# Kernel optimization log

Hardware: AMD Instinct MI355X
Metric: run time of the kernel (lower is better)

The kernel has to match this reference:

```python
import jax, jax.numpy as jnp
import numpy as np

EMBED = 1024
HEADS = 16

def setup_inputs() -> dict:
    key = jax.random.key(0)
    ks = jax.random.split(key, 6)
    N, S = 1, 4096
    half = EMBED // 2
    x = jax.random.normal(ks[0], (N, S, EMBED), dtype=jnp.float32)
    Wq = jax.random.normal(ks[1], (half, half), dtype=jnp.float32) * 0.02
    Wk = jax.random.normal(ks[2], (half, half), dtype=jnp.float32) * 0.02
    Wv = jax.random.normal(ks[3], (half, half), dtype=jnp.float32) * 0.02
    Wo = jax.random.normal(ks[4], (EMBED, half), dtype=jnp.float32) * 0.02
    bo = jnp.zeros((EMBED,), dtype=jnp.float32)
    return {"x": x, "Wq": Wq, "Wk": Wk, "Wv": Wv, "Wo": Wo, "bo": bo}

def reference(x, Wq, Wk, Wv, Wo, bo):
    N, S, E = x.shape
    H = HEADS
    Dh = (E // 2) // H                 # per-head dim of the half-width projections (32)
    scale = float(E // H) ** 0.5       # original scales by head_dim = embed/heads = 64
    left = x[..., : E // 2]            # only the left chunk feeds attention in the source
    # torch Linear: y = x @ W.T (no bias)
    q = (left @ Wq.T).reshape(N, S, H, Dh)
    k = (left @ Wk.T).reshape(N, S, H, Dh)
    v = (left @ Wv.T).reshape(N, S, H, Dh)
    energy = jnp.einsum('nqhd,nkhd->nqkh', q, k)          # [N,S,S,H] full score tensor
    att = jax.nn.softmax(energy / scale, axis=2)          # softmax over key axis
    out = jnp.einsum('nqkh,nkhd->nqhd', att, v)           # [N,S,H,Dh]
    out = out.reshape(N, S, E // 2)
    return out @ Wo.T + bo                                # fc_out: half -> embed
```

## Files before the change

### kernel.cpp

```cpp
#include <hip/hip_runtime.h>
#include <stdint.h>


#define SEQ    4096
#define DMODEL 1024
#define DHALF  512
#define NH     16
#define DH     32

typedef __attribute__((ext_vector_type(4))) float facc4;
typedef __attribute__((ext_vector_type(8))) short bfrag8;

#define MFMA_BF16(a, b, c) __builtin_amdgcn_mfma_f32_16x16x32_bf16((a), (b), (c), 0, 0, 0)

static __device__ __forceinline__ uint16_t f2b(float x) {
    uint32_t u = __float_as_uint(x);
    return (uint16_t)((u + 0x7FFFu + ((u >> 16) & 1u)) >> 16);
}
static __device__ __forceinline__ float b2f(uint16_t b) {
    return __uint_as_float(((uint32_t)b) << 16);
}

static __device__ __forceinline__ bfrag8 cvt8perm(float4 a, float4 b) {
    uint32_t u0 = __float_as_uint(a.x) + 0x8000u, u1 = __float_as_uint(a.y) + 0x8000u;
    uint32_t u2 = __float_as_uint(a.z) + 0x8000u, u3 = __float_as_uint(a.w) + 0x8000u;
    uint32_t u4 = __float_as_uint(b.x) + 0x8000u, u5 = __float_as_uint(b.y) + 0x8000u;
    uint32_t u6 = __float_as_uint(b.z) + 0x8000u, u7 = __float_as_uint(b.w) + 0x8000u;
    union { uint32_t w[4]; bfrag8 r; } u;
    u.w[0] = __builtin_amdgcn_perm(u1, u0, 0x07060302u);
    u.w[1] = __builtin_amdgcn_perm(u3, u2, 0x07060302u);
    u.w[2] = __builtin_amdgcn_perm(u5, u4, 0x07060302u);
    u.w[3] = __builtin_amdgcn_perm(u7, u6, 0x07060302u);
    return u.r;
}

__global__ __launch_bounds__(256) void convert_w(
    const float* __restrict__ Wq, const float* __restrict__ Wk,
    const float* __restrict__ Wv, const float* __restrict__ Wo,
    uint16_t* __restrict__ q, uint16_t* __restrict__ k,
    uint16_t* __restrict__ v, uint16_t* __restrict__ o)
{
    int zz = blockIdx.x;
    const float* src; uint16_t* dst; size_t off;
    if      (zz < 128) { src = Wq; dst = q; off = (size_t)zz * 2048; }
    else if (zz < 256) { src = Wk; dst = k; off = (size_t)(zz - 128) * 2048; }
    else if (zz < 384) { src = Wv; dst = v; off = (size_t)(zz - 256) * 2048; }
    else               { src = Wo; dst = o; off = (size_t)(zz - 384) * 2048; }
    size_t i = off + (size_t)threadIdx.x * 8;
    float4 a = *(const float4*)&src[i];
    float4 b = *(const float4*)&src[i + 4];
    *(bfrag8*)&dst[i] = cvt8perm(a, b);
}

template <int AF32>
__device__ __forceinline__ void gemm128T(
    const void* __restrict__ A, int lda,
    const uint16_t* __restrict__ B, int ldb,
    void* __restrict__ C, int ldc, int cF32,
    const float* __restrict__ bias, float scale,
    int Kd, int m0, int n0)
{
    __shared__ __align__(16) uint16_t As[2][128 * 40];
    __shared__ __align__(16) uint16_t Bs[2][128 * 40];

    const int tid  = threadIdx.x;
    const int lane = tid & 63;
    const int wv   = tid >> 6;
    const int lo   = lane & 15;
    const int quad = lane >> 4;
    const int srow = tid >> 2;
    const int skq  = (tid & 3) * 8;
    const int rb   = (wv >> 1) * 64;
    const int cb   = (wv & 1) * 64;

    const facc4 ZACC = {0.f, 0.f, 0.f, 0.f};
    facc4 acc[4][4];
#pragma unroll
    for (int i = 0; i < 4; ++i)
#pragma unroll
        for (int j = 0; j < 4; ++j) acc[i][j] = ZACC;

    const float*    fA0 = AF32 ? &((const float*)A)[(size_t)(m0 + srow) * lda + skq] : nullptr;
    const float*    fA1 = AF32 ? &((const float*)A)[(size_t)(m0 + srow + 64) * lda + skq] : nullptr;
    const uint16_t* hA0 = AF32 ? nullptr : &((const uint16_t*)A)[(size_t)(m0 + srow) * lda + skq];
    const uint16_t* hA1 = AF32 ? nullptr : &((const uint16_t*)A)[(size_t)(m0 + srow + 64) * lda + skq];
    const uint16_t* pB0 = &B[(size_t)(n0 + srow) * ldb + skq];
    const uint16_t* pB1 = &B[(size_t)(n0 + srow + 64) * ldb + skq];

    bfrag8 ra0, ra1;
    float4 f0a, f0b, f1a, f1b;
    if (AF32) {
        f0a = *(const float4*)fA0; f0b = *(const float4*)(fA0 + 4);
        f1a = *(const float4*)fA1; f1b = *(const float4*)(fA1 + 4);
    } else {
        ra0 = *(const bfrag8*)hA0;
        ra1 = *(const bfrag8*)hA1;
    }
    bfrag8 rb0 = *(const bfrag8*)pB0;
    bfrag8 rb1 = *(const bfrag8*)pB1;

    if (AF32) {
        *(bfrag8*)&As[0][srow * 40 + skq]        = cvt8perm(f0a, f0b);
        *(bfrag8*)&As[0][(srow + 64) * 40 + skq] = cvt8perm(f1a, f1b);
    } else {
        *(bfrag8*)&As[0][srow * 40 + skq]        = ra0;
        *(bfrag8*)&As[0][(srow + 64) * 40 + skq] = ra1;
    }
    *(bfrag8*)&Bs[0][srow * 40 + skq]        = rb0;
    *(bfrag8*)&Bs[0][(srow + 64) * 40 + skq] = rb1;
    __syncthreads();

    int p = 0;
    for (int kt = 0; kt < Kd; kt += 32) {
        const bool more = (kt + 32 < Kd);
        if (more) {
            if (AF32) {
                f0a = *(const float4*)(fA0 + kt + 32); f0b = *(const float4*)(fA0 + kt + 36);
                f1a = *(const float4*)(fA1 + kt + 32); f1b = *(const float4*)(fA1 + kt + 36);
            } else {
                ra0 = *(const bfrag8*)(hA0 + kt + 32);
                ra1 = *(const bfrag8*)(hA1 + kt + 32);
            }
            rb0 = *(const bfrag8*)(pB0 + kt + 32);
            rb1 = *(const bfrag8*)(pB1 + kt + 32);
        }

        bfrag8 af[4], bf[4];
#pragma unroll
        for (int i = 0; i < 4; ++i) {
            af[i] = *(const bfrag8*)&As[p][(rb + i * 16 + lo) * 40 + quad * 8];
            bf[i] = *(const bfrag8*)&Bs[p][(cb + i * 16 + lo) * 40 + quad * 8];
        }
#pragma unroll
        for (int i = 0; i < 4; ++i)
#pragma unroll
            for (int j = 0; j < 4; ++j)
                acc[i][j] = MFMA_BF16(af[i], bf[j], acc[i][j]);

        if (more) {
            if (AF32) {
                *(bfrag8*)&As[1 - p][srow * 40 + skq]        = cvt8perm(f0a, f0b);
                *(bfrag8*)&As[1 - p][(srow + 64) * 40 + skq] = cvt8perm(f1a, f1b);
            } else {
                *(bfrag8*)&As[1 - p][srow * 40 + skq]        = ra0;
                *(bfrag8*)&As[1 - p][(srow + 64) * 40 + skq] = ra1;
            }
            *(bfrag8*)&Bs[1 - p][srow * 40 + skq]        = rb0;
            *(bfrag8*)&Bs[1 - p][(srow + 64) * 40 + skq] = rb1;
            __syncthreads();
            p ^= 1;
        }
    }

#pragma unroll
    for (int j = 0; j < 4; ++j) {
        int col  = n0 + cb + j * 16 + lo;
        float bv = bias ? bias[col] : 0.f;
#pragma unroll
        for (int i = 0; i < 4; ++i) {
#pragma unroll
            for (int r = 0; r < 4; ++r) {
                int row = m0 + rb + i * 16 + quad * 4 + r;
                float v = acc[i][j][r] * scale + bv;
                if (cF32) ((float*)C)[(size_t)row * ldc + col] = v;
                else      ((uint16_t*)C)[(size_t)row * ldc + col] = f2b(v);
            }
        }
    }
}

#define SC_Q (0.125f * 1.4426950408889634f)

__global__ __launch_bounds__(256, 2) void qkv_kernel(
    const float* __restrict__ x,
    const uint16_t* __restrict__ Wqb, const uint16_t* __restrict__ Wkb,
    const uint16_t* __restrict__ Wvb,
    uint16_t* __restrict__ Q, uint16_t* __restrict__ K, uint16_t* __restrict__ V)
{
    const int z = blockIdx.z;
    const uint16_t* W = (z == 0) ? Wqb : (z == 1) ? Wkb : Wvb;
    uint16_t* Out     = (z == 0) ? Q   : (z == 1) ? K   : V;
    float scale       = (z == 0) ? SC_Q : 1.0f;
    gemm128T<1>(x, DMODEL, W, DHALF, Out, DHALF, 0, nullptr, scale, DHALF,
                blockIdx.y * 128, blockIdx.x * 128);
}

__global__ __launch_bounds__(256, 2) void outproj_kernel(
    const uint16_t* __restrict__ O, const uint16_t* __restrict__ Wob,
    const float* __restrict__ bo, float* __restrict__ Y)
{
    gemm128T<0>(O, DHALF, Wob, DHALF, Y, DMODEL, 1, bo, 1.0f, DHALF,
                blockIdx.y * 128, blockIdx.x * 128);
}

__global__ __launch_bounds__(256) void attn_kernel(
    const uint16_t* __restrict__ Q, const uint16_t* __restrict__ Kb,
    const uint16_t* __restrict__ Vb, uint16_t* __restrict__ Op,
    float* __restrict__ lbuf, int kspan)
{
    __shared__ __align__(16) uint16_t Ks[64 * 40];
    __shared__ __align__(16) uint16_t Vt[32 * 64];
    __shared__ __align__(16) uint16_t Ps[4 * 16 * 72];

    const int tid  = threadIdx.x;
    const int lane = tid & 63;
    const int wv   = tid >> 6;
    const int lo   = lane & 15;
    const int quad = lane >> 4;
    const int h    = blockIdx.y;
    const int q0   = blockIdx.x * 64;
    const int sp   = blockIdx.z;
    const int srow = tid >> 2;
    const int skq  = (tid & 3) * 8;

    const facc4 ZACC = {0.f, 0.f, 0.f, 0.f};

    const bfrag8 qf = *(const bfrag8*)&Q[(size_t)(q0 + wv * 16 + lo) * DHALF + h * DH + quad * 8];

    bfrag8 ones;
#pragma unroll
    for (int j = 0; j < 8; ++j) ones[j] = (short)0x3F80;

    int vt_w[8];
#pragma unroll
    for (int j = 0; j < 8; ++j) {
        int d  = skq + j;
        int Rd = ((d & 7) + 2 * (d >> 3)) & 7;
        vt_w[j] = d * 64 + ((((srow >> 3) + Rd) & 7) << 3) + (srow & 7);
    }
    int vt_r[2][2];
#pragma unroll
    for (int dt = 0; dt < 2; ++dt) {
        int d  = dt * 16 + lo;
        int Rd = ((d & 7) + 2 * (d >> 3)) & 7;
#pragma unroll
        for (int c = 0; c < 2; ++c)
            vt_r[c][dt] = d * 64 + ((((c * 4 + quad) + Rd) & 7) << 3);
    }
    const int pbase = wv * (16 * 72);
    const int ps_w  = pbase + lo * 72 + 4 * quad;
    const int ps_r  = pbase + lo * 72 + quad * 8;
    const int ks_r  = lo * 40 + quad * 8;

    const uint16_t* pK = &Kb[(size_t)srow * DHALF + h * DH + skq];
    const uint16_t* pV = &Vb[(size_t)srow * DHALF + h * DH + skq];

    facc4 oacc[2], oaccL;
    oacc[0] = ZACC; oacc[1] = ZACC; oaccL = ZACC;

    const int kb0  = sp * kspan;
    const int kend = kb0 + kspan;

    float4 kreg = *(const float4*)(pK + (size_t)kb0 * DHALF);
    float4 vreg = *(const float4*)(pV + (size_t)kb0 * DHALF);

    for (int kb = kb0; kb < kend; kb += 64) {
        *(float4*)&Ks[srow * 40 + skq] = kreg;
        {
            const uint16_t* vp = (const uint16_t*)&vreg;
#pragma unroll
            for (int j = 0; j < 8; ++j) Vt[vt_w[j]] = vp[j];
        }
        __syncthreads();

        if (kb + 64 < kend) {
            kreg = *(const float4*)(pK + (size_t)(kb + 64) * DHALF);
            vreg = *(const float4*)(pV + (size_t)(kb + 64) * DHALF);
        }

#pragma unroll
        for (int t = 0; t < 4; ++t) {
            bfrag8 kf = *(const bfrag8*)&Ks[t * 640 + ks_r];
            facc4 s = MFMA_BF16(kf, qf, ZACC);
            float p0 = __builtin_amdgcn_exp2f(s[0]);
            float p1 = __builtin_amdgcn_exp2f(s[1]);
            float p2 = __builtin_amdgcn_exp2f(s[2]);
            float p3 = __builtin_amdgcn_exp2f(s[3]);
            uint32_t u0 = __float_as_uint(p0) + 0x8000u;
            uint32_t u1 = __float_as_uint(p1) + 0x8000u;
            uint32_t u2 = __float_as_uint(p2) + 0x8000u;
            uint32_t u3 = __float_as_uint(p3) + 0x8000u;
            uint2 w;
            w.x = __builtin_amdgcn_perm(u1, u0, 0x07060302u);
            w.y = __builtin_amdgcn_perm(u3, u2, 0x07060302u);
            *(uint2*)&Ps[ps_w + 16 * t] = w;
        }
        __builtin_amdgcn_wave_barrier();

#pragma unroll
        for (int c = 0; c < 2; ++c) {
            bfrag8 pf = *(const bfrag8*)&Ps[ps_r + c * 32];
#pragma unroll
            for (int dt = 0; dt < 2; ++dt) {
                bfrag8 vf = *(const bfrag8*)&Vt[vt_r[c][dt]];
                oacc[dt] = MFMA_BF16(pf, vf, oacc[dt]);
            }
            oaccL = MFMA_BF16(pf, ones, oaccL);
        }
        __syncthreads();
    }

    if (lo == 0) {
#pragma unroll
        for (int r = 0; r < 4; ++r)
            lbuf[((size_t)sp * NH + h) * SEQ + q0 + wv * 16 + quad * 4 + r] = oaccL[r];
    }

    uint16_t* Od = Op + (size_t)sp * SEQ * DHALF;
#pragma unroll
    for (int r = 0; r < 4; ++r) {
        int row = q0 + wv * 16 + quad * 4 + r;
        Od[(size_t)row * DHALF + h * DH + lo]      = f2b(oacc[0][r]);
        Od[(size_t)row * DHALF + h * DH + 16 + lo] = f2b(oacc[1][r]);
    }
}

__global__ __launch_bounds__(256) void combine_kernel(
    const uint16_t* __restrict__ Op, const float* __restrict__ lbuf,
    uint16_t* __restrict__ O, int ns)
{
    int t   = blockIdx.x * 256 + threadIdx.x;
    int row = t >> 6;
    int cb  = (t & 63) << 3;
    int h   = cb >> 5;
    float l = 0.f;
    float acc[8] = {0.f, 0.f, 0.f, 0.f, 0.f, 0.f, 0.f, 0.f};
    for (int sp = 0; sp < ns; ++sp) {
        l += lbuf[((size_t)sp * NH + h) * SEQ + row];
        bfrag8 a = *(const bfrag8*)&Op[(size_t)sp * SEQ * DHALF + (size_t)row * DHALF + cb];
#pragma unroll
        for (int j = 0; j < 8; ++j) acc[j] += b2f((uint16_t)a[j]);
    }
    float inv = 1.0f / l;
    bfrag8 o;
#pragma unroll
    for (int j = 0; j < 8; ++j) o[j] = (short)f2b(acc[j] * inv);
    *(bfrag8*)&O[(size_t)row * DHALF + cb] = o;
}

extern "C" void kernel_launch(void* const* d_in, const int* in_sizes, int n_in,
                              void* d_out, int out_size, void* d_ws, size_t ws_size,
                              hipStream_t stream)
{
    const float* x  = (const float*)d_in[0];
    const float* Wq = (const float*)d_in[1];
    const float* Wk = (const float*)d_in[2];
    const float* Wv = (const float*)d_in[3];
    const float* Wo = (const float*)d_in[4];
    const float* bo = (const float*)d_in[5];

    size_t fixed_e = 3 * (size_t)DHALF * DHALF + (size_t)DMODEL * DHALF
                   + 4 * (size_t)SEQ * DHALF;
    size_t need4 = (fixed_e + 4 * (size_t)SEQ * DHALF) * 2
                 + 4 * (size_t)NH * SEQ * 4;
    const int ns = (ws_size >= need4) ? 4 : 2;

    uint16_t* Wqb = (uint16_t*)d_ws;
    uint16_t* Wkb = Wqb + (size_t)DHALF * DHALF;
    uint16_t* Wvb = Wkb + (size_t)DHALF * DHALF;
    uint16_t* Wob = Wvb + (size_t)DHALF * DHALF;
    uint16_t* Q   = Wob + (size_t)DMODEL * DHALF;
    uint16_t* K   = Q + (size_t)SEQ * DHALF;
    uint16_t* V   = K + (size_t)SEQ * DHALF;
    uint16_t* O   = V + (size_t)SEQ * DHALF;
    uint16_t* Op  = O + (size_t)SEQ * DHALF;
    float*  lbuf  = (float*)(Op + (size_t)ns * SEQ * DHALF);

    convert_w<<<640, 256, 0, stream>>>(Wq, Wk, Wv, Wo, Wqb, Wkb, Wvb, Wob);
    qkv_kernel<<<dim3(DHALF / 128, SEQ / 128, 3), 256, 0, stream>>>(
        x, Wqb, Wkb, Wvb, Q, K, V);
    attn_kernel<<<dim3(SEQ / 64, NH, ns), 256, 0, stream>>>(Q, K, V, Op, lbuf, SEQ / ns);
    combine_kernel<<<1024, 256, 0, stream>>>(Op, lbuf, O, ns);
    outproj_kernel<<<dim3(DMODEL / 128, SEQ / 128), 256, 0, stream>>>(
        O, Wob, bo, (float*)d_out);
}
```

Baseline: 194.5 us.

## Fuse weight conversion and split-K combine into the GEMM tile loaders

Removes the separate weight-conversion kernel by loading fp32 weights directly in the GEMMs and converting them to bf16 while staging to shared memory. Removes the combine kernel by having the output-projection GEMM sum the split attention partials and normalize them by the summed softmax denominators as it stages its A tiles. This saves two launches and the intermediate O buffer. In exchange, the fp32 weight loads double B traffic per tile, and the combine work is redone by every column block of the output GEMM (8 times) inside its staging path.

```diff
diff --git a/kernel.cpp b/kernel.cpp
--- a/kernel.cpp
+++ b/kernel.cpp
@@ -34,31 +34,14 @@
     return u.r;
 }
 
-__global__ __launch_bounds__(256) void convert_w(
-    const float* __restrict__ Wq, const float* __restrict__ Wk,
-    const float* __restrict__ Wv, const float* __restrict__ Wo,
-    uint16_t* __restrict__ q, uint16_t* __restrict__ k,
-    uint16_t* __restrict__ v, uint16_t* __restrict__ o)
-{
-    int zz = blockIdx.x;
-    const float* src; uint16_t* dst; size_t off;
-    if      (zz < 128) { src = Wq; dst = q; off = (size_t)zz * 2048; }
-    else if (zz < 256) { src = Wk; dst = k; off = (size_t)(zz - 128) * 2048; }
-    else if (zz < 384) { src = Wv; dst = v; off = (size_t)(zz - 256) * 2048; }
-    else               { src = Wo; dst = o; off = (size_t)(zz - 384) * 2048; }
-    size_t i = off + (size_t)threadIdx.x * 8;
-    float4 a = *(const float4*)&src[i];
-    float4 b = *(const float4*)&src[i + 4];
-    *(bfrag8*)&dst[i] = cvt8perm(a, b);
-}
-
-template <int AF32>
+template <int AMODE, int BF32>
 __device__ __forceinline__ void gemm128T(
     const void* __restrict__ A, int lda,
-    const uint16_t* __restrict__ B, int ldb,
+    const void* __restrict__ B, int ldb,
     void* __restrict__ C, int ldc, int cF32,
     const float* __restrict__ bias, float scale,
-    int Kd, int m0, int n0)
+    int Kd, int m0, int n0,
+    const float* __restrict__ lbuf, int ns)
 {
     __shared__ __align__(16) uint16_t As[2][128 * 40];
     __shared__ __align__(16) uint16_t Bs[2][128 * 40];
@@ -80,50 +63,82 @@
 #pragma unroll
         for (int j = 0; j < 4; ++j) acc[i][j] = ZACC;
 
-    const float*    fA0 = AF32 ? &((const float*)A)[(size_t)(m0 + srow) * lda + skq] : nullptr;
-    const float*    fA1 = AF32 ? &((const float*)A)[(size_t)(m0 + srow + 64) * lda + skq] : nullptr;
-    const uint16_t* hA0 = AF32 ? nullptr : &((const uint16_t*)A)[(size_t)(m0 + srow) * lda + skq];
-    const uint16_t* hA1 = AF32 ? nullptr : &((const uint16_t*)A)[(size_t)(m0 + srow + 64) * lda + skq];
-    const uint16_t* pB0 = &B[(size_t)(n0 + srow) * ldb + skq];
-    const uint16_t* pB1 = &B[(size_t)(n0 + srow + 64) * ldb + skq];
-
-    bfrag8 ra0, ra1;
-    float4 f0a, f0b, f1a, f1b;
-    if (AF32) {
-        f0a = *(const float4*)fA0; f0b = *(const float4*)(fA0 + 4);
-        f1a = *(const float4*)fA1; f1b = *(const float4*)(fA1 + 4);
-    } else {
-        ra0 = *(const bfrag8*)hA0;
-        ra1 = *(const bfrag8*)hA1;
-    }
-    bfrag8 rb0 = *(const bfrag8*)pB0;
-    bfrag8 rb1 = *(const bfrag8*)pB1;
-
-    if (AF32) {
-        *(bfrag8*)&As[0][srow * 40 + skq]        = cvt8perm(f0a, f0b);
-        *(bfrag8*)&As[0][(srow + 64) * 40 + skq] = cvt8perm(f1a, f1b);
-    } else {
-        *(bfrag8*)&As[0][srow * 40 + skq]        = ra0;
-        *(bfrag8*)&As[0][(srow + 64) * 40 + skq] = ra1;
-    }
-    *(bfrag8*)&Bs[0][srow * 40 + skq]        = rb0;
-    *(bfrag8*)&Bs[0][(srow + 64) * 40 + skq] = rb1;
+    bfrag8 a_b[2]; float4 a_f[2][2];
+    bfrag8 b_b[2]; float4 b_f[2][2];
+
+    auto fetchA = [&](int kt) {
+        if constexpr (AMODE == 0) {
+#pragma unroll
+            for (int hf = 0; hf < 2; ++hf)
+                a_b[hf] = *(const bfrag8*)&((const uint16_t*)A)
+                    [(size_t)(m0 + srow + hf * 64) * lda + kt + skq];
+        } else if constexpr (AMODE == 1) {
+#pragma unroll
+            for (int hf = 0; hf < 2; ++hf) {
+                const float* p = &((const float*)A)
+                    [(size_t)(m0 + srow + hf * 64) * lda + kt + skq];
+                a_f[hf][0] = *(const float4*)p;
+                a_f[hf][1] = *(const float4*)(p + 4);
+            }
+        }
+    };
+    auto fetchB = [&](int kt) {
+#pragma unroll
+        for (int hf = 0; hf < 2; ++hf) {
+            if constexpr (BF32) {
+                const float* p = &((const float*)B)
+                    [(size_t)(n0 + srow + hf * 64) * ldb + kt + skq];
+                b_f[hf][0] = *(const float4*)p;
+                b_f[hf][1] = *(const float4*)(p + 4);
+            } else {
+                b_b[hf] = *(const bfrag8*)&((const uint16_t*)B)
+                    [(size_t)(n0 + srow + hf * 64) * ldb + kt + skq];
+            }
+        }
+    };
+    auto stage = [&](int kt, int buf) {
+#pragma unroll
+        for (int hf = 0; hf < 2; ++hf) {
+            bfrag8 av;
+            if constexpr (AMODE == 0) {
+                av = a_b[hf];
+            } else if constexpr (AMODE == 1) {
+                av = cvt8perm(a_f[hf][0], a_f[hf][1]);
+            } else {
+                size_t row = (size_t)(m0 + srow + hf * 64);
+                int h = kt >> 5;
+                float s[8] = {0.f,0.f,0.f,0.f,0.f,0.f,0.f,0.f};
+                float l = 0.f;
+                for (int sp = 0; sp < ns; ++sp) {
+                    bfrag8 v = *(const bfrag8*)&((const uint16_t*)A)
+                        [(size_t)sp * SEQ * DHALF + row * lda + kt + skq];
+                    l += lbuf[((size_t)sp * NH + h) * SEQ + row];
+#pragma unroll
+                    for (int j = 0; j < 8; ++j) s[j] += b2f((uint16_t)v[j]);
+                }
+                float inv = 1.0f / l;
+                float4 x0 = {s[0]*inv, s[1]*inv, s[2]*inv, s[3]*inv};
+                float4 x1 = {s[4]*inv, s[5]*inv, s[6]*inv, s[7]*inv};
+                av = cvt8perm(x0, x1);
+            }
+            *(bfrag8*)&As[buf][(srow + hf * 64) * 40 + skq] = av;
+
+            bfrag8 bv;
+            if constexpr (BF32) bv = cvt8perm(b_f[hf][0], b_f[hf][1]);
+            else                bv = b_b[hf];
+            *(bfrag8*)&Bs[buf][(srow + hf * 64) * 40 + skq] = bv;
+        }
+    };
+
+    fetchA(0);
+    fetchB(0);
+    stage(0, 0);
     __syncthreads();
 
     int p = 0;
     for (int kt = 0; kt < Kd; kt += 32) {
         const bool more = (kt + 32 < Kd);
-        if (more) {
-            if (AF32) {
-                f0a = *(const float4*)(fA0 + kt + 32); f0b = *(const float4*)(fA0 + kt + 36);
-                f1a = *(const float4*)(fA1 + kt + 32); f1b = *(const float4*)(fA1 + kt + 36);
-            } else {
-                ra0 = *(const bfrag8*)(hA0 + kt + 32);
-                ra1 = *(const bfrag8*)(hA1 + kt + 32);
-            }
-            rb0 = *(const bfrag8*)(pB0 + kt + 32);
-            rb1 = *(const bfrag8*)(pB1 + kt + 32);
-        }
+        if (more) { fetchA(kt + 32); fetchB(kt + 32); }
 
         bfrag8 af[4], bf[4];
 #pragma unroll
@@ -138,15 +153,7 @@
                 acc[i][j] = MFMA_BF16(af[i], bf[j], acc[i][j]);
 
         if (more) {
-            if (AF32) {
-                *(bfrag8*)&As[1 - p][srow * 40 + skq]        = cvt8perm(f0a, f0b);
-                *(bfrag8*)&As[1 - p][(srow + 64) * 40 + skq] = cvt8perm(f1a, f1b);
-            } else {
-                *(bfrag8*)&As[1 - p][srow * 40 + skq]        = ra0;
-                *(bfrag8*)&As[1 - p][(srow + 64) * 40 + skq] = ra1;
-            }
-            *(bfrag8*)&Bs[1 - p][srow * 40 + skq]        = rb0;
-            *(bfrag8*)&Bs[1 - p][(srow + 64) * 40 + skq] = rb1;
+            stage(kt + 32, 1 - p);
             __syncthreads();
             p ^= 1;
         }
@@ -173,24 +180,25 @@
 
 __global__ __launch_bounds__(256, 2) void qkv_kernel(
     const float* __restrict__ x,
-    const uint16_t* __restrict__ Wqb, const uint16_t* __restrict__ Wkb,
-    const uint16_t* __restrict__ Wvb,
+    const float* __restrict__ Wq, const float* __restrict__ Wk,
+    const float* __restrict__ Wv,
     uint16_t* __restrict__ Q, uint16_t* __restrict__ K, uint16_t* __restrict__ V)
 {
     const int z = blockIdx.z;
-    const uint16_t* W = (z == 0) ? Wqb : (z == 1) ? Wkb : Wvb;
-    uint16_t* Out     = (z == 0) ? Q   : (z == 1) ? K   : V;
-    float scale       = (z == 0) ? SC_Q : 1.0f;
-    gemm128T<1>(x, DMODEL, W, DHALF, Out, DHALF, 0, nullptr, scale, DHALF,
-                blockIdx.y * 128, blockIdx.x * 128);
+    const float* W = (z == 0) ? Wq : (z == 1) ? Wk : Wv;
+    uint16_t* Out  = (z == 0) ? Q  : (z == 1) ? K  : V;
+    float scale    = (z == 0) ? SC_Q : 1.0f;
+    gemm128T<1, 1>(x, DMODEL, W, DHALF, Out, DHALF, 0, nullptr, scale, DHALF,
+                   blockIdx.y * 128, blockIdx.x * 128, nullptr, 0);
 }
 
 __global__ __launch_bounds__(256, 2) void outproj_kernel(
-    const uint16_t* __restrict__ O, const uint16_t* __restrict__ Wob,
-    const float* __restrict__ bo, float* __restrict__ Y)
-{
-    gemm128T<0>(O, DHALF, Wob, DHALF, Y, DMODEL, 1, bo, 1.0f, DHALF,
-                blockIdx.y * 128, blockIdx.x * 128);
+    const uint16_t* __restrict__ Op, const float* __restrict__ Wo,
+    const float* __restrict__ bo, float* __restrict__ Y,
+    const float* __restrict__ lbuf, int ns)
+{
+    gemm128T<2, 1>(Op, DHALF, Wo, DHALF, Y, DMODEL, 1, bo, 1.0f, DHALF,
+                   blockIdx.y * 128, blockIdx.x * 128, lbuf, ns);
 }
 
 __global__ __launch_bounds__(256) void attn_kernel(
@@ -315,29 +323,6 @@
     }
 }
 
-__global__ __launch_bounds__(256) void combine_kernel(
-    const uint16_t* __restrict__ Op, const float* __restrict__ lbuf,
-    uint16_t* __restrict__ O, int ns)
-{
-    int t   = blockIdx.x * 256 + threadIdx.x;
-    int row = t >> 6;
-    int cb  = (t & 63) << 3;
-    int h   = cb >> 5;
-    float l = 0.f;
-    float acc[8] = {0.f, 0.f, 0.f, 0.f, 0.f, 0.f, 0.f, 0.f};
-    for (int sp = 0; sp < ns; ++sp) {
-        l += lbuf[((size_t)sp * NH + h) * SEQ + row];
-        bfrag8 a = *(const bfrag8*)&Op[(size_t)sp * SEQ * DHALF + (size_t)row * DHALF + cb];
-#pragma unroll
-        for (int j = 0; j < 8; ++j) acc[j] += b2f((uint16_t)a[j]);
-    }
-    float inv = 1.0f / l;
-    bfrag8 o;
-#pragma unroll
-    for (int j = 0; j < 8; ++j) o[j] = (short)f2b(acc[j] * inv);
-    *(bfrag8*)&O[(size_t)row * DHALF + cb] = o;
-}
-
 extern "C" void kernel_launch(void* const* d_in, const int* in_sizes, int n_in,
                               void* d_out, int out_size, void* d_ws, size_t ws_size,
                               hipStream_t stream)
@@ -349,28 +334,18 @@
     const float* Wo = (const float*)d_in[4];
     const float* bo = (const float*)d_in[5];
 
-    size_t fixed_e = 3 * (size_t)DHALF * DHALF + (size_t)DMODEL * DHALF
-                   + 4 * (size_t)SEQ * DHALF;
-    size_t need4 = (fixed_e + 4 * (size_t)SEQ * DHALF) * 2
-                 + 4 * (size_t)NH * SEQ * 4;
+    size_t need4 = (3 + 4) * (size_t)SEQ * DHALF * 2 + 4 * (size_t)NH * SEQ * 4;
     const int ns = (ws_size >= need4) ? 4 : 2;
 
-    uint16_t* Wqb = (uint16_t*)d_ws;
-    uint16_t* Wkb = Wqb + (size_t)DHALF * DHALF;
-    uint16_t* Wvb = Wkb + (size_t)DHALF * DHALF;
-    uint16_t* Wob = Wvb + (size_t)DHALF * DHALF;
-    uint16_t* Q   = Wob + (size_t)DMODEL * DHALF;
-    uint16_t* K   = Q + (size_t)SEQ * DHALF;
-    uint16_t* V   = K + (size_t)SEQ * DHALF;
-    uint16_t* O   = V + (size_t)SEQ * DHALF;
-    uint16_t* Op  = O + (size_t)SEQ * DHALF;
-    float*  lbuf  = (float*)(Op + (size_t)ns * SEQ * DHALF);
-
-    convert_w<<<640, 256, 0, stream>>>(Wq, Wk, Wv, Wo, Wqb, Wkb, Wvb, Wob);
+    uint16_t* Q  = (uint16_t*)d_ws;
+    uint16_t* K  = Q + (size_t)SEQ * DHALF;
+    uint16_t* V  = K + (size_t)SEQ * DHALF;
+    uint16_t* Op = V + (size_t)SEQ * DHALF;
+    float*  lbuf = (float*)(Op + (size_t)ns * SEQ * DHALF);
+
     qkv_kernel<<<dim3(DHALF / 128, SEQ / 128, 3), 256, 0, stream>>>(
-        x, Wqb, Wkb, Wvb, Q, K, V);
+        x, Wq, Wk, Wv, Q, K, V);
     attn_kernel<<<dim3(SEQ / 64, NH, ns), 256, 0, stream>>>(Q, K, V, Op, lbuf, SEQ / ns);
-    combine_kernel<<<1024, 256, 0, stream>>>(Op, lbuf, O, ns);
     outproj_kernel<<<dim3(DMODEL / 128, SEQ / 128), 256, 0, stream>>>(
-        O, Wob, bo, (float*)d_out);
-}
+        Op, Wo, bo, (float*)d_out, lbuf, ns);
+}
```

Result: slower. 228.9 us (+17.7%).
